# Kernel tuning notes

Measured on AMD Instinct MI355X. Metric: run time of the kernel, lower is better.

The kernel has to match this reference:

```python
import jax, jax.numpy as jnp
import numpy as np

N_VERTS = 100000  # vertices per mesh; K = 3*N_VERTS


def det3x3(m):
    # m: [..., 3, 3] closed-form determinant (cheaper than generic LU det)
    a00, a01, a02 = m[..., 0, 0], m[..., 0, 1], m[..., 0, 2]
    a10, a11, a12 = m[..., 1, 0], m[..., 1, 1], m[..., 1, 2]
    a20, a21, a22 = m[..., 2, 0], m[..., 2, 1], m[..., 2, 2]
    return (a00 * (a11 * a22 - a12 * a21)
            - a01 * (a10 * a22 - a12 * a20)
            + a02 * (a10 * a21 - a11 * a20))


def setup_inputs() -> dict:
    key = jax.random.key(0)
    k1, k2 = jax.random.split(key)
    x = jax.random.normal(k1, (64, 3 * N_VERTS), dtype=jnp.float32)
    M = jax.random.randint(k2, (200000, 3), 0, N_VERTS, dtype=jnp.int64)
    return {"x": x, "M": M}


def reference(x, M):
    B = x.shape[0]
    v = x.reshape(B, -1, 3)          # [B, N, 3]
    tets = v[:, M]                    # gather -> [B, T, 3, 3]
    vol = jnp.sum(jnp.abs(det3x3(tets)), axis=1) / 6.0  # [B]
    scale = vol ** (1.0 / 3.0)        # cube root of volume
    out = v / scale[:, None, None]    # broadcast divide
    return out.reshape(x.shape)
```

## Files before the change

### kernel.cpp

```cpp
#include <hip/hip_runtime.h>
#include <hip/hip_fp16.h>


constexpr int NV   = 100000;
constexpr int NT   = 200000;
constexpr int NB   = 64;
constexpr int ROW  = 3 * NV;
constexpr int ROW4 = ROW / 4;

typedef float vfloat4 __attribute__((ext_vector_type(4)));

__global__ __launch_bounds__(256) void transpose_kernel(
    const float* __restrict__ x, __half* __restrict__ xt, float* __restrict__ ws)
{
    __shared__ float tile[64][65];
    if (blockIdx.x == 0 && threadIdx.x < NB) ws[threadIdx.x] = 0.0f;

    const int c0 = blockIdx.x * 64;
    const int c  = threadIdx.x & 63;
    const int b0 = threadIdx.x >> 6;

    if (c0 + c < ROW) {
        #pragma unroll
        for (int k = 0; k < 16; ++k) {
            const int b = b0 + 4 * k;
            tile[c][b] = x[(size_t)b * ROW + c0 + c];
        }
    }
    __syncthreads();

    uint2* outp = (uint2*)(xt + (size_t)c0 * NB);
    #pragma unroll
    for (int k = 0; k < 4; ++k) {
        const int j  = threadIdx.x + k * 256;
        const int cc = j >> 4;
        const int bb = (j & 15) * 4;
        if (c0 + cc < ROW) {
            union { uint2 u; __half2 h[2]; } pk;
            pk.h[0] = __floats2half2_rn(tile[cc][bb],     tile[cc][bb + 1]);
            pk.h[1] = __floats2half2_rn(tile[cc][bb + 2], tile[cc][bb + 3]);
            outp[j] = pk.u;
        }
    }
}

__global__ __launch_bounds__(256, 8) void vol_reduce_kernel(
    const __half* __restrict__ xt,
    const int*    __restrict__ M,
    float*        __restrict__ ws)
{
    const int lane = threadIdx.x & 63;
    const int wib  = threadIdx.x >> 6;
    const int wid  = __builtin_amdgcn_readfirstlane(blockIdx.x * 4 + wib);
    const int nw   = gridDim.x * 4;
    const int chunk = (NT + nw - 1) / nw;
    const int t0 = wid * chunk;
    const int t1 = min(NT, t0 + chunk);

    const __half* __restrict__ base = xt + lane;
    float acc = 0.0f;
    #pragma unroll 4
    for (int t = t0; t < t1; ++t) {
        const int i0 = M[3 * t + 0];
        const int i1 = M[3 * t + 1];
        const int i2 = M[3 * t + 2];
        const __half* p0 = base + (size_t)i0 * 192;
        const __half* p1 = base + (size_t)i1 * 192;
        const __half* p2 = base + (size_t)i2 * 192;
        const float a00 = __half2float(p0[0]);
        const float a01 = __half2float(p0[64]);
        const float a02 = __half2float(p0[128]);
        const float a10 = __half2float(p1[0]);
        const float a11 = __half2float(p1[64]);
        const float a12 = __half2float(p1[128]);
        const float a20 = __half2float(p2[0]);
        const float a21 = __half2float(p2[64]);
        const float a22 = __half2float(p2[128]);
        const float det = a00 * (a11 * a22 - a12 * a21)
                        - a01 * (a10 * a22 - a12 * a20)
                        + a02 * (a10 * a21 - a11 * a20);
        acc += fabsf(det);
    }

    __shared__ float sacc[4][NB];
    sacc[wib][lane] = acc;
    __syncthreads();
    if (threadIdx.x < NB)
        atomicAdd(&ws[threadIdx.x],
                  sacc[0][threadIdx.x] + sacc[1][threadIdx.x] +
                  sacc[2][threadIdx.x] + sacc[3][threadIdx.x]);
}

__global__ __launch_bounds__(256) void scale_kernel(
    const vfloat4* __restrict__ x,
    const float*   __restrict__ ws,
    vfloat4*       __restrict__ out)
{
    const int idx = blockIdx.x * 256 + threadIdx.x;
    const int b   = idx / ROW4;
    const float s = cbrtf(6.0f / ws[b]);
    vfloat4 vv = x[idx];
    vv *= s;
    __builtin_nontemporal_store(vv, &out[idx]);
}

extern "C" void kernel_launch(void* const* d_in, const int* in_sizes, int n_in,
                              void* d_out, int out_size, void* d_ws, size_t ws_size,
                              hipStream_t stream)
{
    const float* x   = (const float*)d_in[0];
    const int*   M   = (const int*)d_in[1];
    float*       out = (float*)d_out;
    float*       ws  = (float*)d_ws;
    __half*      xt  = (__half*)(ws + 256);

    transpose_kernel<<<(ROW + 63) / 64, 256, 0, stream>>>(x, xt, ws);

    vol_reduce_kernel<<<2048, 256, 0, stream>>>(xt, M, ws);

    scale_kernel<<<NB * ROW4 / 256, 256, 0, stream>>>((const vfloat4*)x, ws, (vfloat4*)out);
}
```

Before: 219.8 us.

## Fuse transpose, volume reduction and scaling into one cooperative persistent kernel

Merges the three kernel launches into a single cooperative kernel, using grid-wide syncs between the transpose, the determinant reduction and the scaling phases. The grid is sized from occupancy so it stays persistent, and the transpose and scale phases become grid-stride loops. The reduction loop is manually unrolled by two, issuing all half loads before converting them. This removes launch gaps and tail effects between kernels, at the cost of grid.sync overhead and possibly lower occupancy from the shared tile and the combined register use.

```diff
diff --git a/kernel.cpp b/kernel.cpp
--- a/kernel.cpp
+++ b/kernel.cpp
@@ -1,107 +1,141 @@
 #include <hip/hip_runtime.h>
 #include <hip/hip_fp16.h>
+#include <hip/hip_cooperative_groups.h>
+
+namespace cg = cooperative_groups;
 
 
-constexpr int NV   = 100000;
-constexpr int NT   = 200000;
-constexpr int NB   = 64;
-constexpr int ROW  = 3 * NV;
-constexpr int ROW4 = ROW / 4;
+constexpr int NV    = 100000;
+constexpr int NT    = 200000;
+constexpr int NB    = 64;
+constexpr int ROW   = 3 * NV;
+constexpr int ROW4  = ROW / 4;
+constexpr int TILES = (ROW + 63) / 64;
 
 typedef float vfloat4 __attribute__((ext_vector_type(4)));
 
-__global__ __launch_bounds__(256) void transpose_kernel(
-    const float* __restrict__ x, __half* __restrict__ xt, float* __restrict__ ws)
+__global__ __launch_bounds__(256, 8) void fused_kernel(
+    const float* __restrict__ x,
+    const int*   __restrict__ M,
+    float*       __restrict__ out,
+    float*       __restrict__ ws,
+    __half*      __restrict__ xt)
 {
+    cg::grid_group grid = cg::this_grid();
     __shared__ float tile[64][65];
+
     if (blockIdx.x == 0 && threadIdx.x < NB) ws[threadIdx.x] = 0.0f;
 
-    const int c0 = blockIdx.x * 64;
     const int c  = threadIdx.x & 63;
     const int b0 = threadIdx.x >> 6;
+    for (int tb = blockIdx.x; tb < TILES; tb += gridDim.x) {
+        const int c0 = tb * 64;
+        if (c0 + c < ROW) {
+            #pragma unroll
+            for (int k = 0; k < 16; ++k) {
+                const int b = b0 + 4 * k;
+                tile[c][b] = x[(size_t)b * ROW + c0 + c];
+            }
+        }
+        __syncthreads();
+        uint2* outp = (uint2*)(xt + (size_t)c0 * NB);
+        #pragma unroll
+        for (int k = 0; k < 4; ++k) {
+            const int j  = threadIdx.x + k * 256;
+            const int cc = j >> 4;
+            const int bb = (j & 15) * 4;
+            if (c0 + cc < ROW) {
+                union { uint2 u; __half2 h[2]; } pk;
+                pk.h[0] = __floats2half2_rn(tile[cc][bb],     tile[cc][bb + 1]);
+                pk.h[1] = __floats2half2_rn(tile[cc][bb + 2], tile[cc][bb + 3]);
+                outp[j] = pk.u;
+            }
+        }
+        __syncthreads();
+    }
 
-    if (c0 + c < ROW) {
-        #pragma unroll
-        for (int k = 0; k < 16; ++k) {
-            const int b = b0 + 4 * k;
-            tile[c][b] = x[(size_t)b * ROW + c0 + c];
+    grid.sync();
+
+    {
+        const int lane = threadIdx.x & 63;
+        const int wib  = threadIdx.x >> 6;
+        const int wid  = __builtin_amdgcn_readfirstlane(blockIdx.x * 4 + wib);
+        const int nw   = gridDim.x * 4;
+        const int chunk = (NT + nw - 1) / nw;
+        const int t0 = wid * chunk;
+        const int t1 = min(NT, t0 + chunk);
+
+        const __half* __restrict__ base = xt + lane;
+        float acc = 0.0f;
+        int t = t0;
+        for (; t + 2 <= t1; t += 2) {
+            const int a0 = M[3*t + 0], a1 = M[3*t + 1], a2 = M[3*t + 2];
+            const int c0i = M[3*t + 3], c1 = M[3*t + 4], c2 = M[3*t + 5];
+            const __half* pa0 = base + (size_t)a0  * 192;
+            const __half* pa1 = base + (size_t)a1  * 192;
+            const __half* pa2 = base + (size_t)a2  * 192;
+            const __half* pb0 = base + (size_t)c0i * 192;
+            const __half* pb1 = base + (size_t)c1  * 192;
+            const __half* pb2 = base + (size_t)c2  * 192;
+            const __half ha00 = pa0[0], ha01 = pa0[64], ha02 = pa0[128];
+            const __half ha10 = pa1[0], ha11 = pa1[64], ha12 = pa1[128];
+            const __half ha20 = pa2[0], ha21 = pa2[64], ha22 = pa2[128];
+            const __half hb00 = pb0[0], hb01 = pb0[64], hb02 = pb0[128];
+            const __half hb10 = pb1[0], hb11 = pb1[64], hb12 = pb1[128];
+            const __half hb20 = pb2[0], hb21 = pb2[64], hb22 = pb2[128];
+            {
+                const float A00=__half2float(ha00), A01=__half2float(ha01), A02=__half2float(ha02);
+                const float A10=__half2float(ha10), A11=__half2float(ha11), A12=__half2float(ha12);
+                const float A20=__half2float(ha20), A21=__half2float(ha21), A22=__half2float(ha22);
+                acc += fabsf(A00*(A11*A22 - A12*A21)
+                           - A01*(A10*A22 - A12*A20)
+                           + A02*(A10*A21 - A11*A20));
+            }
+            {
+                const float A00=__half2float(hb00), A01=__half2float(hb01), A02=__half2float(hb02);
+                const float A10=__half2float(hb10), A11=__half2float(hb11), A12=__half2float(hb12);
+                const float A20=__half2float(hb20), A21=__half2float(hb21), A22=__half2float(hb22);
+                acc += fabsf(A00*(A11*A22 - A12*A21)
+                           - A01*(A10*A22 - A12*A20)
+                           + A02*(A10*A21 - A11*A20));
+            }
+        }
+        if (t < t1) {
+            const int i0 = M[3*t + 0], i1 = M[3*t + 1], i2 = M[3*t + 2];
+            const __half* p0 = base + (size_t)i0 * 192;
+            const __half* p1 = base + (size_t)i1 * 192;
+            const __half* p2 = base + (size_t)i2 * 192;
+            const float A00=__half2float(p0[0]), A01=__half2float(p0[64]), A02=__half2float(p0[128]);
+            const float A10=__half2float(p1[0]), A11=__half2float(p1[64]), A12=__half2float(p1[128]);
+            const float A20=__half2float(p2[0]), A21=__half2float(p2[64]), A22=__half2float(p2[128]);
+            acc += fabsf(A00*(A11*A22 - A12*A21)
+                       - A01*(A10*A22 - A12*A20)
+                       + A02*(A10*A21 - A11*A20));
+        }
+
+        float* sacc = &tile[0][0];
+        sacc[wib * NB + lane] = acc;
+        __syncthreads();
+        if (threadIdx.x < NB)
+            atomicAdd(&ws[threadIdx.x],
+                      sacc[0*NB + threadIdx.x] + sacc[1*NB + threadIdx.x] +
+                      sacc[2*NB + threadIdx.x] + sacc[3*NB + threadIdx.x]);
+    }
+
+    grid.sync();
+
+    {
+        const vfloat4* __restrict__ x4 = (const vfloat4*)x;
+        vfloat4*       __restrict__ o4 = (vfloat4*)out;
+        const int total = NB * ROW4;
+        for (int idx = blockIdx.x * 256 + threadIdx.x; idx < total; idx += gridDim.x * 256) {
+            const int b   = idx / ROW4;
+            const float s = cbrtf(6.0f / ws[b]);
+            vfloat4 vv = x4[idx];
+            vv *= s;
+            __builtin_nontemporal_store(vv, &o4[idx]);
         }
     }
-    __syncthreads();
-
-    uint2* outp = (uint2*)(xt + (size_t)c0 * NB);
-    #pragma unroll
-    for (int k = 0; k < 4; ++k) {
-        const int j  = threadIdx.x + k * 256;
-        const int cc = j >> 4;
-        const int bb = (j & 15) * 4;
-        if (c0 + cc < ROW) {
-            union { uint2 u; __half2 h[2]; } pk;
-            pk.h[0] = __floats2half2_rn(tile[cc][bb],     tile[cc][bb + 1]);
-            pk.h[1] = __floats2half2_rn(tile[cc][bb + 2], tile[cc][bb + 3]);
-            outp[j] = pk.u;
-        }
-    }
-}
-
-__global__ __launch_bounds__(256, 8) void vol_reduce_kernel(
-    const __half* __restrict__ xt,
-    const int*    __restrict__ M,
-    float*        __restrict__ ws)
-{
-    const int lane = threadIdx.x & 63;
-    const int wib  = threadIdx.x >> 6;
-    const int wid  = __builtin_amdgcn_readfirstlane(blockIdx.x * 4 + wib);
-    const int nw   = gridDim.x * 4;
-    const int chunk = (NT + nw - 1) / nw;
-    const int t0 = wid * chunk;
-    const int t1 = min(NT, t0 + chunk);
-
-    const __half* __restrict__ base = xt + lane;
-    float acc = 0.0f;
-    #pragma unroll 4
-    for (int t = t0; t < t1; ++t) {
-        const int i0 = M[3 * t + 0];
-        const int i1 = M[3 * t + 1];
-        const int i2 = M[3 * t + 2];
-        const __half* p0 = base + (size_t)i0 * 192;
-        const __half* p1 = base + (size_t)i1 * 192;
-        const __half* p2 = base + (size_t)i2 * 192;
-        const float a00 = __half2float(p0[0]);
-        const float a01 = __half2float(p0[64]);
-        const float a02 = __half2float(p0[128]);
-        const float a10 = __half2float(p1[0]);
-        const float a11 = __half2float(p1[64]);
-        const float a12 = __half2float(p1[128]);
-        const float a20 = __half2float(p2[0]);
-        const float a21 = __half2float(p2[64]);
-        const float a22 = __half2float(p2[128]);
-        const float det = a00 * (a11 * a22 - a12 * a21)
-                        - a01 * (a10 * a22 - a12 * a20)
-                        + a02 * (a10 * a21 - a11 * a20);
-        acc += fabsf(det);
-    }
-
-    __shared__ float sacc[4][NB];
-    sacc[wib][lane] = acc;
-    __syncthreads();
-    if (threadIdx.x < NB)
-        atomicAdd(&ws[threadIdx.x],
-                  sacc[0][threadIdx.x] + sacc[1][threadIdx.x] +
-                  sacc[2][threadIdx.x] + sacc[3][threadIdx.x]);
-}
-
-__global__ __launch_bounds__(256) void scale_kernel(
-    const vfloat4* __restrict__ x,
-    const float*   __restrict__ ws,
-    vfloat4*       __restrict__ out)
-{
-    const int idx = blockIdx.x * 256 + threadIdx.x;
-    const int b   = idx / ROW4;
-    const float s = cbrtf(6.0f / ws[b]);
-    vfloat4 vv = x[idx];
-    vv *= s;
-    __builtin_nontemporal_store(vv, &out[idx]);
 }
 
 extern "C" void kernel_launch(void* const* d_in, const int* in_sizes, int n_in,
@@ -114,9 +148,18 @@
     float*       ws  = (float*)d_ws;
     __half*      xt  = (__half*)(ws + 256);
 
-    transpose_kernel<<<(ROW + 63) / 64, 256, 0, stream>>>(x, xt, ws);
+    static int grid = 0;
+    if (grid == 0) {
+        int perCU = 0, ncu = 0, dev = 0;
+        (void)hipGetDevice(&dev);
+        hipError_t e = hipOccupancyMaxActiveBlocksPerMultiprocessor(&perCU, fused_kernel, 256, 0);
+        (void)hipDeviceGetAttribute(&ncu, hipDeviceAttributeMultiprocessorCount, dev);
+        if (e != hipSuccess || perCU <= 0) perCU = 4;
+        if (ncu <= 0) ncu = 256;
+        const int g = perCU * ncu;
+        grid = g < 2048 ? g : 2048;
+    }
 
-    vol_reduce_kernel<<<2048, 256, 0, stream>>>(xt, M, ws);
-
-    scale_kernel<<<NB * ROW4 / 256, 256, 0, stream>>>((const vfloat4*)x, ws, (vfloat4*)out);
+    void* args[] = { (void*)&x, (void*)&M, (void*)&out, (void*)&ws, (void*)&xt };
+    hipLaunchCooperativeKernel(fused_kernel, dim3(grid), dim3(256), args, 0, stream);
 }
```

Result: slower. 446.4 us (+103.1%).
